# Kernel optimization log

Hardware: AMD Instinct MI355X
Metric: run time of the kernel (lower is better)

## Reference

```python
import jax, jax.numpy as jnp
import numpy as np

# Static problem sizes (see shape_source)
B, SX, SY = 256, 256, 70          # graphs, encoder nodes/graph, decoder nodes/graph
F, EMB, H = 512, 256, 256          # f_size, emb_size, h_size
VOCAB = 256
E = 4 * B * SY                     # 71680 edges
N_SLT = 4                          # SltEdgeTypes
N_SRT = 8                          # len(SrtEdgeTypes)


def setup_inputs() -> dict:
    key = jax.random.key(0)
    ks = jax.random.split(key, 24)
    s = 0.02
    inp = {
        'x': jax.random.normal(ks[0], (B * SX, F), jnp.float32),
        'x_batch': jnp.repeat(jnp.arange(B, dtype=jnp.int64), SX),
        'tgt_y': jax.random.randint(ks[1], (B * SY,), 0, VOCAB, jnp.int64),
        'tgt_edge_index': jax.random.randint(ks[2], (2, E), 0, B * SY, jnp.int64),
        'tgt_edge_type': jax.random.randint(ks[3], (E,), 0, N_SLT, jnp.int64),
        'tgt_y_batch': jnp.repeat(jnp.arange(B, dtype=jnp.int64), SY),
        'embeds': jax.random.normal(ks[4], (VOCAB, EMB), jnp.float32) * s,
    }
    dims = [(EMB, H), (H, H), (H, EMB)]
    k = 5
    for l, (din, dout) in enumerate(dims, start=1):
        inp[f'W_in{l}'] = jax.random.normal(ks[k + 0], (din, dout), jnp.float32) * s
        inp[f'Wq{l}'] = jax.random.normal(ks[k + 1], (dout, F), jnp.float32) * s
        inp[f'Wv{l}'] = jax.random.normal(ks[k + 2], (F, dout), jnp.float32) * s
        inp[f'Ee{l}'] = jax.random.normal(ks[k + 3], (N_SLT, dout), jnp.float32) * s
        k += 4
    inp['lin_z_w'] = jax.random.normal(ks[k], (EMB, VOCAB), jnp.float32) * s
    inp['lin_z_b'] = jnp.zeros((VOCAB,), jnp.float32)
    inp['lin_g_w'] = jax.random.normal(ks[k + 1], (2 * EMB, N_SRT), jnp.float32) * s
    inp['lin_g_b'] = jnp.zeros((N_SRT,), jnp.float32)
    return inp


def gcn_dec_layer(x_b, y, src, tgt, etype, W_in, Wq, Wv, Ee):
    """Edge-type-conditioned message passing + cross-attention onto encoder x.
    x_b: [B,SX,F]; y: [Ny,din]. Returns ([Ny,dout], alpha [B,SY,SX])."""
    h = y @ W_in                                   # [Ny, dout]
    m = h[src] + Ee[etype]                         # gather + type embedding
    agg = jax.ops.segment_sum(m, tgt, num_segments=y.shape[0])
    q = (h @ Wq).reshape(B, SY, F)                 # query into encoder space
    logits = jnp.einsum('bqf,bkf->bqk', q, x_b) / jnp.sqrt(jnp.float32(F))
    alpha = jax.nn.softmax(logits, axis=-1)        # [B,SY,SX]
    ctx = jnp.einsum('bqk,bkf->bqf', alpha, x_b) @ Wv  # [B,SY,dout]
    out = jax.nn.relu(h + agg + ctx.reshape(h.shape[0], -1))
    return out, alpha


def reference(x, x_batch, tgt_y, tgt_edge_index, tgt_edge_type, tgt_y_batch,
              embeds, W_in1, Wq1, Wv1, Ee1, W_in2, Wq2, Wv2, Ee2,
              W_in3, Wq3, Wv3, Ee3, lin_z_w, lin_z_b, lin_g_w, lin_g_b):
    x_b = x.reshape(B, SX, F)
    src, tgt = tgt_edge_index[0], tgt_edge_index[1]
    y = embeds[tgt_y]                              # [Ny, EMB]
    y, a1 = gcn_dec_layer(x_b, y, src, tgt, tgt_edge_type, W_in1, Wq1, Wv1, Ee1)
    y, a2 = gcn_dec_layer(x_b, y, src, tgt, tgt_edge_type, W_in2, Wq2, Wv2, Ee2)
    y, a3 = gcn_dec_layer(x_b, y, src, tgt, tgt_edge_type, W_in3, Wq3, Wv3, Ee3)
    y_score = y @ lin_z_w + lin_z_b                # [Ny, VOCAB]
    ef = y[tgt_edge_index]                         # [2, E, EMB]
    ef = jnp.transpose(ef, (1, 0, 2)).reshape(E, 2 * EMB)
    y_edge_rel_score = ef @ lin_g_w + lin_g_b      # [E, N_SRT]
    return (y, y_score, y_edge_rel_score, a1, a2, a3)
```

## Files before the change

kernel.cpp:

```cpp
#include <hip/hip_runtime.h>
#include <cstddef>
#include <cstdint>

#define B_    256
#define SX_   256
#define SY_   70
#define F_    512
#define EMB_  256
#define NY_   (B_*SY_)
#define NE_   (4*B_*SY_)

typedef short s16x8 __attribute__((ext_vector_type(8)));
typedef float f32x4 __attribute__((ext_vector_type(4)));
typedef unsigned short us4 __attribute__((ext_vector_type(4)));
typedef unsigned short us8 __attribute__((ext_vector_type(8)));

__device__ __forceinline__ unsigned short f2bf(float f) {
    unsigned u = __builtin_bit_cast(unsigned, f);
    u += 0x7fffu + ((u >> 16) & 1u);
    return (unsigned short)(u >> 16);
}
__device__ __forceinline__ float bf2f(unsigned short b) {
    unsigned u = ((unsigned)b) << 16;
    return __builtin_bit_cast(float, u);
}

template<int EPI, int SWZ>
__global__ __launch_bounds__(256, 2)
void gemm_mfma(const unsigned short* __restrict__ A, int lda, long sAb,
               const unsigned short* __restrict__ Bt, int ldb, long sBb,
               float* __restrict__ Cf, int ldc, long sCfb,
               unsigned short* __restrict__ Cb, int ldcb, long sCbb,
               const float* __restrict__ aux1, long sAux,
               int M, int K, float scale, int nx, int ny)
{
    __shared__ unsigned short As[128 * 64];
    __shared__ unsigned short Bs[128 * 64];
    char* AsB = (char*)As;
    char* BsB = (char*)Bs;
    const int tid = threadIdx.x;
    int bxi, byi, z;
    if (SWZ) {
        const int nwg = gridDim.x;
        const int bid = blockIdx.x;
        const int wg = (bid & 7) * (nwg >> 3) + (bid >> 3);
        bxi = wg % nx;
        byi = (wg / nx) % ny;
        z   = wg / (nx * ny);
    } else {
        bxi = blockIdx.x; byi = blockIdx.y; z = blockIdx.z;
    }
    A  += (size_t)z * sAb;
    Bt += (size_t)z * sBb;
    const char* auxp = (const char*)aux1 + (size_t)z * sAux;
    const int bm = byi * 128, bn = bxi * 128;
    const int lane = tid & 63;
    const int w = tid >> 6, wr = w >> 1, wc = w & 1;
    const int l15 = lane & 15, lq = lane >> 4;

    f32x4 acc[4][4];
    const f32x4 z4 = {0.f, 0.f, 0.f, 0.f};
#pragma unroll
    for (int m = 0; m < 4; ++m)
#pragma unroll
        for (int n = 0; n < 4; ++n) acc[m][n] = z4;

    for (int k0 = 0; k0 < K; k0 += 64) {
#pragma unroll
        for (int i = 0; i < 4; ++i) {
            const int row = i * 32 + (tid >> 3);
            const int k8  = (tid & 7) ^ (row & 7);
            int ra = bm + row; ra = (ra < M) ? ra : (M - 1);
            const unsigned short* g = A + (size_t)ra * lda + k0 + k8 * 8;
            __builtin_amdgcn_global_load_lds(
                (const __attribute__((address_space(1))) unsigned int*)g,
                (__attribute__((address_space(3))) unsigned int*)(AsB + i * 4096 + tid * 16),
                16, 0, 0);
        }
#pragma unroll
        for (int i = 0; i < 4; ++i) {
            const int row = i * 32 + (tid >> 3);
            const int k8  = (tid & 7) ^ (row & 7);
            const unsigned short* g = Bt + (size_t)(bn + row) * ldb + k0 + k8 * 8;
            __builtin_amdgcn_global_load_lds(
                (const __attribute__((address_space(1))) unsigned int*)g,
                (__attribute__((address_space(3))) unsigned int*)(BsB + i * 4096 + tid * 16),
                16, 0, 0);
        }
        __syncthreads();
#pragma unroll
        for (int kk = 0; kk < 2; ++kk) {
            s16x8 af[4], bf[4];
#pragma unroll
            for (int m = 0; m < 4; ++m) {
                const int row = wr * 64 + m * 16 + l15;
                const int slot = (kk * 4 + lq) ^ (row & 7);
                af[m] = *(const s16x8*)(AsB + row * 128 + slot * 16);
            }
#pragma unroll
            for (int n = 0; n < 4; ++n) {
                const int col = wc * 64 + n * 16 + l15;
                const int slot = (kk * 4 + lq) ^ (col & 7);
                bf[n] = *(const s16x8*)(BsB + col * 128 + slot * 16);
            }
#pragma unroll
            for (int m = 0; m < 4; ++m)
#pragma unroll
                for (int n = 0; n < 4; ++n)
                    acc[m][n] = __builtin_amdgcn_mfma_f32_16x16x32_bf16(
                        af[m], bf[n], acc[m][n], 0, 0, 0);
        }
        __syncthreads();
    }

    float* cf = Cf ? Cf + (size_t)z * sCfb : nullptr;
    unsigned short* cb = Cb ? Cb + (size_t)z * sCbb : nullptr;
#pragma unroll
    for (int m = 0; m < 4; ++m) {
#pragma unroll
        for (int n = 0; n < 4; ++n) {
            const int col = bn + wc * 64 + n * 16 + l15;
            f32x4 v = acc[m][n];
#pragma unroll
            for (int r = 0; r < 4; ++r) {
                const int gr = bm + wr * 64 + m * 16 + lq * 4 + r;
                if (gr >= M) continue;
                float o = v[r] * scale;
                if (EPI == 4) o += ((const float*)auxp)[col];
                if (EPI == 7) {
                    if (col < 256) cb[(size_t)gr * ldcb + col] = f2bf(o);
                    else ((unsigned short*)cf)[(size_t)gr * 512 + (col - 256)] = f2bf(o);
                } else {
                    if (cf) cf[(size_t)gr * ldc + col] = o;
                    if (cb) cb[(size_t)gr * ldcb + col] = f2bf(o);
                }
            }
        }
    }
}

__global__ __launch_bounds__(512, 1)
void attn_pv(const unsigned short* __restrict__ Q,
             const unsigned short* __restrict__ X,
             const unsigned short* __restrict__ XV,
             long sXVb,
             const unsigned short* __restrict__ aggb,
             float* __restrict__ Aout,
             unsigned short* __restrict__ Yb,
             float* __restrict__ Yf,
             float scale)
{
    __shared__ unsigned short As[128 * 64];
    __shared__ unsigned short Bs[256 * 64];
    __shared__ unsigned short Al[128 * 256];
    __shared__ float red[4][2][64];
    char* AsB = (char*)As;
    char* BsB = (char*)Bs;
    char* AlB = (char*)Al;
    const int tid = threadIdx.x;
    const int z = blockIdx.x;
    const unsigned short* Qb  = Q + (size_t)z * SY_ * F_;
    const unsigned short* Xb  = X + (size_t)z * SX_ * F_;
    const unsigned short* xvb = XV + (size_t)z * sXVb;
    const int lane = tid & 63;
    const int w = tid >> 6, wr = w >> 2, wc = w & 3;
    const int l15 = lane & 15, lq = lane >> 4;

    f32x4 acc[4][4];
    const f32x4 z4 = {0.f, 0.f, 0.f, 0.f};
#pragma unroll
    for (int m = 0; m < 4; ++m)
#pragma unroll
        for (int n = 0; n < 4; ++n) acc[m][n] = z4;

    for (int k0 = 0; k0 < F_; k0 += 64) {
#pragma unroll
        for (int i = 0; i < 2; ++i) {
            const int row = i * 64 + (tid >> 3);
            const int k8  = (tid & 7) ^ (row & 7);
            const int ra = (row < SY_) ? row : (SY_ - 1);
            const unsigned short* g = Qb + (size_t)ra * F_ + k0 + k8 * 8;
            __builtin_amdgcn_global_load_lds(
                (const __attribute__((address_space(1))) unsigned int*)g,
                (__attribute__((address_space(3))) unsigned int*)(AsB + i * 8192 + tid * 16),
                16, 0, 0);
        }
#pragma unroll
        for (int i = 0; i < 4; ++i) {
            const int row = i * 64 + (tid >> 3);
            const int k8  = (tid & 7) ^ (row & 7);
            const unsigned short* g = Xb + (size_t)row * F_ + k0 + k8 * 8;
            __builtin_amdgcn_global_load_lds(
                (const __attribute__((address_space(1))) unsigned int*)g,
                (__attribute__((address_space(3))) unsigned int*)(BsB + i * 8192 + tid * 16),
                16, 0, 0);
        }
        __syncthreads();
#pragma unroll
        for (int kk = 0; kk < 2; ++kk) {
            s16x8 af[4], bf[4];
#pragma unroll
            for (int m = 0; m < 4; ++m) {
                const int row = wr * 64 + m * 16 + l15;
                const int slot = (kk * 4 + lq) ^ (row & 7);
                af[m] = *(const s16x8*)(AsB + row * 128 + slot * 16);
            }
#pragma unroll
            for (int n = 0; n < 4; ++n) {
                const int col = wc * 64 + n * 16 + l15;
                const int slot = (kk * 4 + lq) ^ (col & 7);
                bf[n] = *(const s16x8*)(BsB + col * 128 + slot * 16);
            }
#pragma unroll
            for (int m = 0; m < 4; ++m)
#pragma unroll
                for (int n = 0; n < 4; ++n)
                    acc[m][n] = __builtin_amdgcn_mfma_f32_16x16x32_bf16(
                        af[m], bf[n], acc[m][n], 0, 0, 0);
        }
        __syncthreads();
    }

#pragma unroll
    for (int m = 0; m < 4; ++m)
#pragma unroll
        for (int n = 0; n < 4; ++n)
#pragma unroll
            for (int r = 0; r < 4; ++r) acc[m][n][r] *= scale;

    float rmax[4][4];
#pragma unroll
    for (int m = 0; m < 4; ++m)
#pragma unroll
        for (int r = 0; r < 4; ++r) {
            float mx = acc[m][0][r];
#pragma unroll
            for (int n = 1; n < 4; ++n) mx = fmaxf(mx, acc[m][n][r]);
            mx = fmaxf(mx, __shfl_xor(mx, 1));
            mx = fmaxf(mx, __shfl_xor(mx, 2));
            mx = fmaxf(mx, __shfl_xor(mx, 4));
            mx = fmaxf(mx, __shfl_xor(mx, 8));
            rmax[m][r] = mx;
        }
    if (l15 == 0) {
#pragma unroll
        for (int m = 0; m < 4; ++m)
#pragma unroll
            for (int r = 0; r < 4; ++r)
                red[wc][wr][m * 16 + lq * 4 + r] = rmax[m][r];
    }
    __syncthreads();
    float rtot[4][4];
#pragma unroll
    for (int m = 0; m < 4; ++m)
#pragma unroll
        for (int r = 0; r < 4; ++r) {
            const int lr = m * 16 + lq * 4 + r;
            rtot[m][r] = fmaxf(fmaxf(red[0][wr][lr], red[1][wr][lr]),
                               fmaxf(red[2][wr][lr], red[3][wr][lr]));
        }
    __syncthreads();
    float rsum[4][4];
#pragma unroll
    for (int m = 0; m < 4; ++m)
#pragma unroll
        for (int r = 0; r < 4; ++r) {
            float s = 0.f;
#pragma unroll
            for (int n = 0; n < 4; ++n) {
                float e = __expf(acc[m][n][r] - rtot[m][r]);
                acc[m][n][r] = e;
                s += e;
            }
            s += __shfl_xor(s, 1);
            s += __shfl_xor(s, 2);
            s += __shfl_xor(s, 4);
            s += __shfl_xor(s, 8);
            rsum[m][r] = s;
        }
    if (l15 == 0) {
#pragma unroll
        for (int m = 0; m < 4; ++m)
#pragma unroll
            for (int r = 0; r < 4; ++r)
                red[wc][wr][m * 16 + lq * 4 + r] = rsum[m][r];
    }
    __syncthreads();
    float* ao = Aout + (size_t)z * SY_ * SX_;
#pragma unroll
    for (int m = 0; m < 4; ++m)
#pragma unroll
        for (int r = 0; r < 4; ++r) {
            const int lr = m * 16 + lq * 4 + r;
            const int row = wr * 64 + lr;
            const float inv = 1.0f / (red[0][wr][lr] + red[1][wr][lr] +
                                      red[2][wr][lr] + red[3][wr][lr]);
#pragma unroll
            for (int n = 0; n < 4; ++n) {
                const int col = wc * 64 + n * 16 + l15;
                const float o = acc[m][n][r] * inv;
                if (row < SY_) ao[(size_t)row * SX_ + col] = o;
                *(unsigned short*)(AlB + row * 512 +
                    (((col >> 3) ^ (row & 7)) << 4) + ((col & 7) << 1)) = f2bf(o);
            }
        }
    __syncthreads();

    f32x4 oac[4][4];
#pragma unroll
    for (int m = 0; m < 4; ++m)
#pragma unroll
        for (int n = 0; n < 4; ++n) oac[m][n] = z4;

    for (int ks = 0; ks < 4; ++ks) {
        const int k0 = ks * 64;
#pragma unroll
        for (int i = 0; i < 4; ++i) {
            const int row = i * 64 + (tid >> 3);
            const int k8  = (tid & 7) ^ (row & 7);
            const unsigned short* g = xvb + (size_t)row * 256 + k0 + k8 * 8;
            __builtin_amdgcn_global_load_lds(
                (const __attribute__((address_space(1))) unsigned int*)g,
                (__attribute__((address_space(3))) unsigned int*)(BsB + i * 8192 + tid * 16),
                16, 0, 0);
        }
        __syncthreads();
#pragma unroll
        for (int kk = 0; kk < 2; ++kk) {
            s16x8 af[4], bf[4];
#pragma unroll
            for (int m = 0; m < 4; ++m) {
                const int row = wr * 64 + m * 16 + l15;
                const int chunk = (k0 >> 3) + kk * 4 + lq;
                af[m] = *(const s16x8*)(AlB + row * 512 + ((chunk ^ (row & 7)) << 4));
            }
#pragma unroll
            for (int n = 0; n < 4; ++n) {
                const int col = wc * 64 + n * 16 + l15;
                const int slot = (kk * 4 + lq) ^ (col & 7);
                bf[n] = *(const s16x8*)(BsB + col * 128 + slot * 16);
            }
#pragma unroll
            for (int m = 0; m < 4; ++m)
#pragma unroll
                for (int n = 0; n < 4; ++n)
                    oac[m][n] = __builtin_amdgcn_mfma_f32_16x16x32_bf16(
                        af[m], bf[n], oac[m][n], 0, 0, 0);
        }
        __syncthreads();
    }

#pragma unroll
    for (int m = 0; m < 4; ++m)
#pragma unroll
        for (int n = 0; n < 4; ++n) {
            const int col = wc * 64 + n * 16 + l15;
            f32x4 v = oac[m][n];
#pragma unroll
            for (int r = 0; r < 4; ++r) {
                const int row = wr * 64 + m * 16 + lq * 4 + r;
                if (row >= SY_) continue;
                const size_t node = (size_t)z * SY_ + row;
                float o = v[r] + bf2f(aggb[node * 256 + col]);
                o = fmaxf(o, 0.f);
                Yb[node * 256 + col] = f2bf(o);
                if (Yf) Yf[node * 256 + col] = o;
            }
        }
}

__global__ __launch_bounds__(256)
void conv_x(const float* __restrict__ in, unsigned short* __restrict__ out, int n8)
{
    for (int i = blockIdx.x * 256 + threadIdx.x; i < n8; i += 2048 * 256) {
        float4 a = ((const float4*)in)[i * 2];
        float4 b = ((const float4*)in)[i * 2 + 1];
        us8 o = { f2bf(a.x), f2bf(a.y), f2bf(a.z), f2bf(a.w),
                  f2bf(b.x), f2bf(b.y), f2bf(b.z), f2bf(b.w) };
        ((us8*)out)[i] = o;
    }
}

struct WAll {
    const float* src[10];
    unsigned short* dst[10];
    int R[10];
    int C[10];
};

__global__ __launch_bounds__(256)
void conv_wT_all(WAll d)
{
    const int z = blockIdx.z;
    const int R = d.R[z], C = d.C[z];
    const int c0 = blockIdx.x * 64, r0 = blockIdx.y * 64;
    if (c0 >= C || r0 >= R) return;
    const float* in = d.src[z];
    unsigned short* outT = d.dst[z];
    __shared__ unsigned short t[64][65];
    const int r = threadIdx.x >> 4, cq = (threadIdx.x & 15) << 2;
#pragma unroll
    for (int i = 0; i < 4; ++i) {
        const int rr = r + i * 16;
        float4 v = *(const float4*)(in + (size_t)(r0 + rr) * C + c0 + cq);
        t[rr][cq + 0] = f2bf(v.x); t[rr][cq + 1] = f2bf(v.y);
        t[rr][cq + 2] = f2bf(v.z); t[rr][cq + 3] = f2bf(v.w);
    }
    __syncthreads();
    const int c = threadIdx.x >> 2, sq = (threadIdx.x & 3) << 4;
    us8 o0, o1;
#pragma unroll
    for (int i = 0; i < 8; ++i) { o0[i] = t[sq + i][c]; o1[i] = t[sq + 8 + i][c]; }
    *(us8*)(outT + (size_t)(c0 + c) * R + r0 + sq) = o0;
    *(us8*)(outT + (size_t)(c0 + c) * R + r0 + sq + 8) = o1;
}

__global__ __launch_bounds__(256)
void gather_embed(const float* __restrict__ embeds, const int* __restrict__ tgt_y,
                  unsigned short* __restrict__ yb)
{
    const int i = blockIdx.x * 8 + (threadIdx.x >> 5);
    const int c8 = (threadIdx.x & 31) * 8;
    const int v = tgt_y[i];
    const float* p = embeds + (size_t)v * 256 + c8;
    float4 a = *(const float4*)p;
    float4 b = *(const float4*)(p + 4);
    us8 o = { f2bf(a.x), f2bf(a.y), f2bf(a.z), f2bf(a.w),
              f2bf(b.x), f2bf(b.y), f2bf(b.z), f2bf(b.w) };
    *(us8*)(yb + (size_t)i * 256 + c8) = o;
}

__global__ __launch_bounds__(256)
void edge_deg(const int* __restrict__ tgt, int* __restrict__ deg)
{
    const int e = blockIdx.x * 256 + threadIdx.x;
    if (e < NE_) atomicAdd(&deg[tgt[e]], 1);
}

__global__ __launch_bounds__(1024)
void scan_off(const int* __restrict__ deg, int* __restrict__ off, int* __restrict__ cursor)
{
    __shared__ int ls[1024];
    const int t = threadIdx.x;
    const int base = t * 18;
    int local[18];
    int s = 0;
#pragma unroll
    for (int i = 0; i < 18; ++i) {
        const int idx = base + i;
        const int v = (idx < NY_) ? deg[idx] : 0;
        local[i] = s; s += v;
    }
    ls[t] = s;
    __syncthreads();
    for (int d = 1; d < 1024; d <<= 1) {
        int v = (t >= d) ? ls[t - d] : 0;
        __syncthreads();
        ls[t] += v;
        __syncthreads();
    }
    const int excl = (t == 0) ? 0 : ls[t - 1];
#pragma unroll
    for (int i = 0; i < 18; ++i) {
        const int idx = base + i;
        if (idx < NY_) {
            const int o = excl + local[i];
            off[idx] = o; cursor[idx] = o;
        }
    }
    if (t == 1023) off[NY_] = ls[1023];
}

__global__ __launch_bounds__(256)
void edge_fill(const int* __restrict__ tgt, int* __restrict__ cursor,
               int* __restrict__ elist)
{
    const int e = blockIdx.x * 256 + threadIdx.x;
    if (e >= NE_) return;
    const int pos = atomicAdd(&cursor[tgt[e]], 1);
    elist[pos] = e;
}

__global__ __launch_bounds__(256)
void node_agg(const unsigned short* __restrict__ hb,
              const float* __restrict__ Ee,
              const int* __restrict__ src, const int* __restrict__ etype,
              const int* __restrict__ off, const int* __restrict__ elist,
              unsigned short* __restrict__ aggb)
{
    const int nid  = blockIdx.x * 4 + (threadIdx.x >> 6);
    const int lane = threadIdx.x & 63;
    const int c = lane * 4;
    const int k0 = off[nid], k1 = off[nid + 1];
    us4 sv = *(const us4*)(hb + (size_t)nid * 256 + c);
    float4 acc;
    acc.x = bf2f(sv[0]); acc.y = bf2f(sv[1]);
    acc.z = bf2f(sv[2]); acc.w = bf2f(sv[3]);
    int cnt0 = 0, cnt1 = 0, cnt2 = 0, cnt3 = 0;
    for (int k = k0; k < k1; ++k) {
        const int e = elist[k];
        const int sfrom = src[e];
        const int ty = etype[e];
        us4 hv = *(const us4*)(hb + (size_t)sfrom * 256 + c);
        acc.x += bf2f(hv[0]); acc.y += bf2f(hv[1]);
        acc.z += bf2f(hv[2]); acc.w += bf2f(hv[3]);
        cnt0 += (ty == 0); cnt1 += (ty == 1); cnt2 += (ty == 2); cnt3 += (ty == 3);
    }
    float4 e0 = *(const float4*)(Ee + c);
    float4 e1 = *(const float4*)(Ee + 256 + c);
    float4 e2 = *(const float4*)(Ee + 512 + c);
    float4 e3 = *(const float4*)(Ee + 768 + c);
    acc.x += cnt0 * e0.x + cnt1 * e1.x + cnt2 * e2.x + cnt3 * e3.x;
    acc.y += cnt0 * e0.y + cnt1 * e1.y + cnt2 * e2.y + cnt3 * e3.y;
    acc.z += cnt0 * e0.z + cnt1 * e1.z + cnt2 * e2.z + cnt3 * e3.z;
    acc.w += cnt0 * e0.w + cnt1 * e1.w + cnt2 * e2.w + cnt3 * e3.w;
    us4 o = { f2bf(acc.x), f2bf(acc.y), f2bf(acc.z), f2bf(acc.w) };
    *(us4*)(aggb + (size_t)nid * 256 + c) = o;
}

__global__ __launch_bounds__(256)
void edge_w(const float* __restrict__ y, const float* __restrict__ W,
            float* __restrict__ Y12)
{
    __shared__ float Ws[4096];
    __shared__ float ys[16][260];
    const int tid = threadIdx.x;
#pragma unroll
    for (int i = 0; i < 4; ++i)
        ((float4*)Ws)[i * 256 + tid] = ((const float4*)W)[i * 256 + tid];
    const int r = tid >> 4, seg = tid & 15;
    const int r0 = blockIdx.x * 16;
#pragma unroll
    for (int i = 0; i < 4; ++i) {
        const int c4 = seg + i * 16;
        *(float4*)&ys[r][c4 * 4] = *(const float4*)(y + (size_t)(r0 + r) * 256 + c4 * 4);
    }
    __syncthreads();
    const int j = tid & 15;
    const int row = tid >> 4;
    const float* Wcol = Ws + ((j < 8) ? j : (2048 + j - 8));
    float acc = 0.f;
#pragma unroll 4
    for (int c = 0; c < 256; ++c) acc = fmaf(ys[row][c], Wcol[c * 8], acc);
    Y12[(size_t)(r0 + row) * 16 + j] = acc;
}

__global__ __launch_bounds__(256)
void edge_gather(const float* __restrict__ Y12, const int* __restrict__ src,
                 const int* __restrict__ tgt, const float* __restrict__ bias,
                 float* __restrict__ esc)
{
    const int e = blockIdx.x * 256 + threadIdx.x;
    if (e >= NE_) return;
    const float* a = Y12 + (size_t)src[e] * 16;
    const float* b = Y12 + (size_t)tgt[e] * 16 + 8;
    float4 a0 = ((const float4*)a)[0], a1 = ((const float4*)a)[1];
    float4 b0 = ((const float4*)b)[0], b1 = ((const float4*)b)[1];
    float4 c0 = ((const float4*)bias)[0], c1 = ((const float4*)bias)[1];
    float4 o0, o1;
    o0.x = a0.x + b0.x + c0.x; o0.y = a0.y + b0.y + c0.y;
    o0.z = a0.z + b0.z + c0.z; o0.w = a0.w + b0.w + c0.w;
    o1.x = a1.x + b1.x + c1.x; o1.y = a1.y + b1.y + c1.y;
    o1.z = a1.z + b1.z + c1.z; o1.w = a1.w + b1.w + c1.w;
    ((float4*)(esc + (size_t)e * 8))[0] = o0;
    ((float4*)(esc + (size_t)e * 8))[1] = o1;
}

extern "C" void kernel_launch(void* const* d_in, const int* in_sizes, int n_in,
                              void* d_out, int out_size, void* d_ws, size_t ws_size,
                              hipStream_t stream)
{
    const float* x       = (const float*)d_in[0];
    const int*   tgt_y   = (const int*)d_in[2];
    const int*   eidx    = (const int*)d_in[3];
    const int*   etype   = (const int*)d_in[4];
    const float* embeds  = (const float*)d_in[6];
    const float* W_in[3] = {(const float*)d_in[7],  (const float*)d_in[11], (const float*)d_in[15]};
    const float* Wq[3]   = {(const float*)d_in[8],  (const float*)d_in[12], (const float*)d_in[16]};
    const float* Wv[3]   = {(const float*)d_in[9],  (const float*)d_in[13], (const float*)d_in[17]};
    const float* Ee[3]   = {(const float*)d_in[10], (const float*)d_in[14], (const float*)d_in[18]};
    const float* lin_z_w = (const float*)d_in[19];
    const float* lin_z_b = (const float*)d_in[20];
    const float* lin_g_w = (const float*)d_in[21];
    const float* lin_g_b = (const float*)d_in[22];
    const int* src = eidx;
    const int* tgt = eidx + NE_;

    float* out = (float*)d_out;
    float* y_final = out;
    float* score   = out + 4587520;
    float* esc     = out + 9175040;
    float* aout[3] = {out + 9748480, out + 14336000, out + 18923520};

    char* wsb = (char*)d_ws;
    unsigned short* xb     = (unsigned short*)(wsb + 0);
    unsigned short* xvTall = (unsigned short*)(wsb + 67108864);
    unsigned short* hb     = (unsigned short*)(wsb + 167772160);
    unsigned short* aggb   = (unsigned short*)(wsb + 176947200);
    unsigned short* qb     = (unsigned short*)(wsb + 186122240);
    unsigned short* yb     = (unsigned short*)(wsb + 204472320);
    char* wt = wsb + 213647360;
    unsigned short* wcatT[3], *wqT[3], *wvT[3];
    for (int l = 0; l < 3; ++l) {
        wcatT[l] = (unsigned short*)(wt + l * 393216);
        wqT[l]   = (unsigned short*)(wt + 1179648 + l * 262144);
        wvT[l]   = (unsigned short*)(wt + 1966080 + l * 262144);
    }
    unsigned short* lzT = (unsigned short*)(wt + 2752512);
    char* extra = wsb + 216530944;
    float* Y12    = (float*)extra;
    int*   deg    = (int*)(extra + 1146880);
    int*   off    = (int*)(extra + 1218560);
    int*   cursor = (int*)(extra + 1290244);
    int*   elist  = (int*)(extra + 1361924);

    hipMemsetAsync(deg, 0, NY_ * sizeof(int), stream);
    edge_deg<<<280, 256, 0, stream>>>(tgt, deg);
    scan_off<<<1, 1024, 0, stream>>>(deg, off, cursor);
    edge_fill<<<280, 256, 0, stream>>>(tgt, cursor, elist);

    conv_x<<<2048, 256, 0, stream>>>(x, xb, 4194304);
    WAll wd;
    for (int l = 0; l < 3; ++l) {
        wd.src[l]     = W_in[l]; wd.dst[l]     = wcatT[l]; wd.R[l]     = 256; wd.C[l]     = 256;
        wd.src[3 + l] = Wq[l];   wd.dst[3 + l] = wqT[l];   wd.R[3 + l] = 256; wd.C[3 + l] = 512;
        wd.src[6 + l] = Wv[l];   wd.dst[6 + l] = wvT[l];   wd.R[6 + l] = 512; wd.C[6 + l] = 256;
    }
    wd.src[9] = lin_z_w; wd.dst[9] = lzT; wd.R[9] = 256; wd.C[9] = 256;
    conv_wT_all<<<dim3(8, 8, 10), 256, 0, stream>>>(wd);
    gather_embed<<<2240, 256, 0, stream>>>(embeds, tgt_y, yb);

    gemm_mfma<0, 0><<<dim3(2, 4, 3), 256, 0, stream>>>(
        wqT[0], 256, 131072L,  wcatT[0], 256, 196608L,
        nullptr, 0, 0,  wcatT[0] + 65536, 256, 196608L,
        nullptr, 0, 512, 256, 1.f, 0, 0);

    gemm_mfma<0, 1><<<3072, 256, 0, stream>>>(
        wvT[0], 512, 0,  xb, 512, (long)SX_ * F_,
        nullptr, 0, 0,  xvTall, 256, 768L * 256,
        nullptr, 0, 768, 512, 1.f, 2, 6);

    const float qscale = 0.044194173824159216f;
    for (int l = 0; l < 3; ++l) {
        gemm_mfma<7, 0><<<dim3(6, 140, 1), 256, 0, stream>>>(
            yb, 256, 0,  wcatT[l], 256, 0,
            (float*)qb, 512, 0,  hb, 256, 0,
            nullptr, 0, NY_, 256, 1.f, 0, 0);
        node_agg<<<4480, 256, 0, stream>>>(hb, Ee[l], src, etype, off, elist, aggb);
        attn_pv<<<256, 512, 0, stream>>>(
            qb, xb, xvTall + (size_t)l * 65536, 768L * 256,
            aggb, aout[l], yb, (l == 2) ? y_final : nullptr, qscale);
    }
    gemm_mfma<4, 0><<<dim3(2, 140, 1), 256, 0, stream>>>(
        yb, 256, 0,  lzT, 256, 0,
        score, 256, 0,  nullptr, 0, 0,
        lin_z_b, 0, NY_, 256, 1.f, 0, 0);
    edge_w<<<1120, 256, 0, stream>>>(y_final, lin_g_w, Y12);
    edge_gather<<<280, 256, 0, stream>>>(Y12, src, tgt, lin_g_b, esc);
}
```

Measured before the change: 449.0 us.

## Fuse edge aggregation into attention kernel and lin_z projection into last layer

The separate node_agg kernel is removed. Each attention block now gathers and sums its own graph's 70 decoder nodes' neighbour messages into shared memory before the QK loop, so the aggregate never goes through global memory. For the final layer, a templated epilogue writes the bf16 output rows into LDS and runs the lin_z GEMM plus bias there, which replaces the standalone score GEMM launch. This cuts kernel launches and global round trips. In exchange, LDS use per block rises and an irregular, latency-bound gather is serialized inside a kernel that runs one block per CU.

```diff
diff --git a/kernel.cpp b/kernel.cpp
--- a/kernel.cpp
+++ b/kernel.cpp
@@ -139,20 +139,28 @@
     }
 }
 
+template<int LAST>
 __global__ __launch_bounds__(512, 1)
 void attn_pv(const unsigned short* __restrict__ Q,
              const unsigned short* __restrict__ X,
              const unsigned short* __restrict__ XV,
              long sXVb,
-             const unsigned short* __restrict__ aggb,
+             const unsigned short* __restrict__ hb,
+             const float* __restrict__ Ee,
+             const int* __restrict__ srcI, const int* __restrict__ etype,
+             const int* __restrict__ off,  const int* __restrict__ elist,
+             const unsigned short* __restrict__ lzT,
+             const float* __restrict__ lzb,
              float* __restrict__ Aout,
              unsigned short* __restrict__ Yb,
              float* __restrict__ Yf,
+             float* __restrict__ Score,
              float scale)
 {
     __shared__ unsigned short As[128 * 64];
     __shared__ unsigned short Bs[256 * 64];
     __shared__ unsigned short Al[128 * 256];
+    __shared__ char aggL[70 * 520];
     __shared__ float red[4][2][64];
     char* AsB = (char*)As;
     char* BsB = (char*)Bs;
@@ -166,6 +174,37 @@
     const int w = tid >> 6, wr = w >> 2, wc = w & 3;
     const int l15 = lane & 15, lq = lane >> 4;
 
+    {
+        const int c = lane * 4;
+        for (int n = w; n < SY_; n += 8) {
+            const int g = z * SY_ + n;
+            const int k0 = off[g], k1 = off[g + 1];
+            us4 sv = *(const us4*)(hb + (size_t)g * 256 + c);
+            float4 a4;
+            a4.x = bf2f(sv[0]); a4.y = bf2f(sv[1]);
+            a4.z = bf2f(sv[2]); a4.w = bf2f(sv[3]);
+            int c0 = 0, c1 = 0, c2 = 0, c3 = 0;
+            for (int k = k0; k < k1; ++k) {
+                const int e = elist[k];
+                const int ty = etype[e];
+                us4 hv = *(const us4*)(hb + (size_t)srcI[e] * 256 + c);
+                a4.x += bf2f(hv[0]); a4.y += bf2f(hv[1]);
+                a4.z += bf2f(hv[2]); a4.w += bf2f(hv[3]);
+                c0 += (ty == 0); c1 += (ty == 1); c2 += (ty == 2); c3 += (ty == 3);
+            }
+            float4 e0 = *(const float4*)(Ee + c);
+            float4 e1 = *(const float4*)(Ee + 256 + c);
+            float4 e2 = *(const float4*)(Ee + 512 + c);
+            float4 e3 = *(const float4*)(Ee + 768 + c);
+            a4.x += c0 * e0.x + c1 * e1.x + c2 * e2.x + c3 * e3.x;
+            a4.y += c0 * e0.y + c1 * e1.y + c2 * e2.y + c3 * e3.y;
+            a4.z += c0 * e0.z + c1 * e1.z + c2 * e2.z + c3 * e3.z;
+            a4.w += c0 * e0.w + c1 * e1.w + c2 * e2.w + c3 * e3.w;
+            us4 o = { f2bf(a4.x), f2bf(a4.y), f2bf(a4.z), f2bf(a4.w) };
+            *(us4*)(aggL + n * 520 + c * 2) = o;
+        }
+    }
+
     f32x4 acc[4][4];
     const f32x4 z4 = {0.f, 0.f, 0.f, 0.f};
 #pragma unroll
@@ -361,12 +400,74 @@
                 const int row = wr * 64 + m * 16 + lq * 4 + r;
                 if (row >= SY_) continue;
                 const size_t node = (size_t)z * SY_ + row;
-                float o = v[r] + bf2f(aggb[node * 256 + col]);
+                float o = v[r] + bf2f(*(const unsigned short*)(aggL + row * 520 + col * 2));
                 o = fmaxf(o, 0.f);
-                Yb[node * 256 + col] = f2bf(o);
+                const unsigned short ob = f2bf(o);
+                Yb[node * 256 + col] = ob;
                 if (Yf) Yf[node * 256 + col] = o;
-            }
-        }
+                if (LAST)
+                    *(unsigned short*)(AlB + row * 512 +
+                        (((col >> 3) ^ (row & 7)) << 4) + ((col & 7) << 1)) = ob;
+            }
+        }
+
+    if (LAST) {
+        __syncthreads();
+#pragma unroll
+        for (int m = 0; m < 4; ++m)
+#pragma unroll
+            for (int n = 0; n < 4; ++n) oac[m][n] = z4;
+        for (int ks = 0; ks < 4; ++ks) {
+            const int k0 = ks * 64;
+#pragma unroll
+            for (int i = 0; i < 4; ++i) {
+                const int row = i * 64 + (tid >> 3);
+                const int k8  = (tid & 7) ^ (row & 7);
+                const unsigned short* g = lzT + (size_t)row * 256 + k0 + k8 * 8;
+                __builtin_amdgcn_global_load_lds(
+                    (const __attribute__((address_space(1))) unsigned int*)g,
+                    (__attribute__((address_space(3))) unsigned int*)(BsB + i * 8192 + tid * 16),
+                    16, 0, 0);
+            }
+            __syncthreads();
+#pragma unroll
+            for (int kk = 0; kk < 2; ++kk) {
+                s16x8 af[4], bf[4];
+#pragma unroll
+                for (int m = 0; m < 4; ++m) {
+                    const int row = wr * 64 + m * 16 + l15;
+                    const int chunk = (k0 >> 3) + kk * 4 + lq;
+                    af[m] = *(const s16x8*)(AlB + row * 512 + ((chunk ^ (row & 7)) << 4));
+                }
+#pragma unroll
+                for (int n = 0; n < 4; ++n) {
+                    const int col = wc * 64 + n * 16 + l15;
+                    const int slot = (kk * 4 + lq) ^ (col & 7);
+                    bf[n] = *(const s16x8*)(BsB + col * 128 + slot * 16);
+                }
+#pragma unroll
+                for (int m = 0; m < 4; ++m)
+#pragma unroll
+                    for (int n = 0; n < 4; ++n)
+                        oac[m][n] = __builtin_amdgcn_mfma_f32_16x16x32_bf16(
+                            af[m], bf[n], oac[m][n], 0, 0, 0);
+            }
+            __syncthreads();
+        }
+#pragma unroll
+        for (int m = 0; m < 4; ++m)
+#pragma unroll
+            for (int n = 0; n < 4; ++n) {
+                const int col = wc * 64 + n * 16 + l15;
+                f32x4 v = oac[m][n];
+#pragma unroll
+                for (int r = 0; r < 4; ++r) {
+                    const int row = wr * 64 + m * 16 + lq * 4 + r;
+                    if (row >= SY_) continue;
+                    Score[((size_t)z * SY_ + row) * 256 + col] = v[r] + lzb[col];
+                }
+            }
+    }
 }
 
 __global__ __launch_bounds__(256)
@@ -479,43 +580,6 @@
     if (e >= NE_) return;
     const int pos = atomicAdd(&cursor[tgt[e]], 1);
     elist[pos] = e;
-}
-
-__global__ __launch_bounds__(256)
-void node_agg(const unsigned short* __restrict__ hb,
-              const float* __restrict__ Ee,
-              const int* __restrict__ src, const int* __restrict__ etype,
-              const int* __restrict__ off, const int* __restrict__ elist,
-              unsigned short* __restrict__ aggb)
-{
-    const int nid  = blockIdx.x * 4 + (threadIdx.x >> 6);
-    const int lane = threadIdx.x & 63;
-    const int c = lane * 4;
-    const int k0 = off[nid], k1 = off[nid + 1];
-    us4 sv = *(const us4*)(hb + (size_t)nid * 256 + c);
-    float4 acc;
-    acc.x = bf2f(sv[0]); acc.y = bf2f(sv[1]);
-    acc.z = bf2f(sv[2]); acc.w = bf2f(sv[3]);
-    int cnt0 = 0, cnt1 = 0, cnt2 = 0, cnt3 = 0;
-    for (int k = k0; k < k1; ++k) {
-        const int e = elist[k];
-        const int sfrom = src[e];
-        const int ty = etype[e];
-        us4 hv = *(const us4*)(hb + (size_t)sfrom * 256 + c);
-        acc.x += bf2f(hv[0]); acc.y += bf2f(hv[1]);
-        acc.z += bf2f(hv[2]); acc.w += bf2f(hv[3]);
-        cnt0 += (ty == 0); cnt1 += (ty == 1); cnt2 += (ty == 2); cnt3 += (ty == 3);
-    }
-    float4 e0 = *(const float4*)(Ee + c);
-    float4 e1 = *(const float4*)(Ee + 256 + c);
-    float4 e2 = *(const float4*)(Ee + 512 + c);
-    float4 e3 = *(const float4*)(Ee + 768 + c);
-    acc.x += cnt0 * e0.x + cnt1 * e1.x + cnt2 * e2.x + cnt3 * e3.x;
-    acc.y += cnt0 * e0.y + cnt1 * e1.y + cnt2 * e2.y + cnt3 * e3.y;
-    acc.z += cnt0 * e0.z + cnt1 * e1.z + cnt2 * e2.z + cnt3 * e3.z;
-    acc.w += cnt0 * e0.w + cnt1 * e1.w + cnt2 * e2.w + cnt3 * e3.w;
-    us4 o = { f2bf(acc.x), f2bf(acc.y), f2bf(acc.z), f2bf(acc.w) };
-    *(us4*)(aggb + (size_t)nid * 256 + c) = o;
 }
 
 __global__ __launch_bounds__(256)
@@ -596,7 +660,6 @@
     unsigned short* xb     = (unsigned short*)(wsb + 0);
     unsigned short* xvTall = (unsigned short*)(wsb + 67108864);
     unsigned short* hb     = (unsigned short*)(wsb + 167772160);
-    unsigned short* aggb   = (unsigned short*)(wsb + 176947200);
     unsigned short* qb     = (unsigned short*)(wsb + 186122240);
     unsigned short* yb     = (unsigned short*)(wsb + 204472320);
     char* wt = wsb + 213647360;
@@ -646,15 +709,20 @@
             yb, 256, 0,  wcatT[l], 256, 0,
             (float*)qb, 512, 0,  hb, 256, 0,
             nullptr, 0, NY_, 256, 1.f, 0, 0);
-        node_agg<<<4480, 256, 0, stream>>>(hb, Ee[l], src, etype, off, elist, aggb);
-        attn_pv<<<256, 512, 0, stream>>>(
-            qb, xb, xvTall + (size_t)l * 65536, 768L * 256,
-            aggb, aout[l], yb, (l == 2) ? y_final : nullptr, qscale);
-    }
-    gemm_mfma<4, 0><<<dim3(2, 140, 1), 256, 0, stream>>>(
-        yb, 256, 0,  lzT, 256, 0,
-        score, 256, 0,  nullptr, 0, 0,
-        lin_z_b, 0, NY_, 256, 1.f, 0, 0);
+        if (l < 2) {
+            attn_pv<0><<<256, 512, 0, stream>>>(
+                qb, xb, xvTall + (size_t)l * 65536, 768L * 256,
+                hb, Ee[l], src, etype, off, elist,
+                nullptr, nullptr,
+                aout[l], yb, nullptr, nullptr, qscale);
+        } else {
+            attn_pv<1><<<256, 512, 0, stream>>>(
+                qb, xb, xvTall + (size_t)l * 65536, 768L * 256,
+                hb, Ee[l], src, etype, off, elist,
+                lzT, lin_z_b,
+                aout[l], yb, y_final, score, qscale);
+        }
+    }
     edge_w<<<1120, 256, 0, stream>>>(y_final, lin_g_w, Y12);
     edge_gather<<<280, 256, 0, stream>>>(Y12, src, tgt, lin_g_b, esc);
 }
```

Result: slower. 474.5 us (+5.7%).
